# Optimization experiments

Measured on AMD Instinct MI355X. Metric: run time of the kernel, lower is better.

The kernel has to match this reference:

```python
import jax, jax.numpy as jnp
import numpy as np
import math

NH, NKV, D = 32, 8, 128  # query heads, kv heads, head_dim
ROPE_THETA = 10000.0


def _rotate_half(x):
    x1, x2 = jnp.split(x, 2, axis=-1)
    return jnp.concatenate([-x2, x1], axis=-1)


def _rope_cache(position_ids):
    # position_ids: [B, S] int -> cos, sin: [B, S, D]
    inv_freq = 1.0 / (ROPE_THETA ** (jnp.arange(0, D, 2, dtype=jnp.float32) / D))
    freqs = position_ids.astype(jnp.float32)[..., None] * inv_freq  # [B,S,D/2]
    emb = jnp.concatenate([freqs, freqs], axis=-1)  # [B,S,D]
    return jnp.cos(emb), jnp.sin(emb)


def setup_inputs() -> dict:
    key = jax.random.key(0)
    k0, k1, k2, k3, k4 = jax.random.split(key, 5)
    B, S, H = 1, 2048, 4096
    scale = 0.02
    return {
        "hidden_states": jax.random.normal(k0, (B, S, H), jnp.float32),
        "position_ids": jnp.broadcast_to(jnp.arange(S, dtype=jnp.int32), (B, S)),
        "Wq": jax.random.normal(k1, (H, NH * D), jnp.float32) * scale,
        "Wk": jax.random.normal(k2, (H, NKV * D), jnp.float32) * scale,
        "Wv": jax.random.normal(k3, (H, NKV * D), jnp.float32) * scale,
        "Wo": jax.random.normal(k4, (NH * D, H), jnp.float32) * scale,
    }


def reference(hidden_states, position_ids, Wq, Wk, Wv, Wo):
    B, S, H = hidden_states.shape
    # QKV projections, move heads front: [B, H, S, D]
    Q = (hidden_states @ Wq).reshape(B, S, NH, D).transpose(0, 2, 1, 3)
    K = (hidden_states @ Wk).reshape(B, S, NKV, D).transpose(0, 2, 1, 3)
    V = (hidden_states @ Wv).reshape(B, S, NKV, D).transpose(0, 2, 1, 3)
    # RoPE
    cos, sin = _rope_cache(position_ids)  # [B,S,D]
    cos, sin = cos[:, None], sin[:, None]  # broadcast over heads
    Q = Q * cos + _rotate_half(Q) * sin
    K = K * cos + _rotate_half(K) * sin
    # GQA: repeat kv heads to match query heads
    g = NH // NKV
    K = jnp.repeat(K, g, axis=1)
    V = jnp.repeat(V, g, axis=1)
    # scaled QK^T with causal mask (mask=True -> keep, else finfo.min)
    scores = jnp.einsum("bhqd,bhkd->bhqk", Q, K) / math.sqrt(D)
    causal = jnp.tril(jnp.ones((S, S), dtype=bool))
    scores = jnp.where(causal, scores, jnp.finfo(scores.dtype).min)
    probs = jax.nn.softmax(scores.astype(jnp.float32), axis=-1).astype(Q.dtype)
    attn = jnp.einsum("bhqk,bhkd->bhqd", probs, V)
    attn = attn.transpose(0, 2, 1, 3).reshape(B, S, NH * D)
    return attn @ Wo
```

## Files before the change

### kernel.cpp

```cpp
#include <hip/hip_runtime.h>
#include <hip/hip_bf16.h>
#include <math.h>

typedef __bf16 bf16;
typedef __bf16 bf16x4 __attribute__((ext_vector_type(4)));
typedef __bf16 bf16x8 __attribute__((ext_vector_type(8)));
typedef float f32x4 __attribute__((ext_vector_type(4)));

#define GLB __attribute__((address_space(1)))
#define LDSAS __attribute__((address_space(3)))

__global__ void probe_dtype(const unsigned int* __restrict__ X, int* __restrict__ flag) {
  int t = threadIdx.x;
  int cnt = 0;
  for (int i = t; i < 512; i += 64) {
    unsigned int e = (X[i] >> 7) & 0xFF;
    cnt += (e >= 110 && e <= 135) ? 1 : 0;
  }
#pragma unroll
  for (int off = 32; off > 0; off >>= 1) cnt += __shfl_down(cnt, off, 64);
  if (t == 0) flag[0] = (cnt < 256) ? 1 : 0;
}

__global__ void prep_weights(const void* __restrict__ Wq, const void* __restrict__ Wk,
                             const void* __restrict__ Wv, const void* __restrict__ Wo,
                             const void* __restrict__ X,
                             bf16* __restrict__ Wqkvt, bf16* __restrict__ Wot,
                             bf16* __restrict__ Xb, const int* __restrict__ flag) {
  const int f = flag[0];
  const int t = threadIdx.x;
  int b = blockIdx.x;
  __shared__ __attribute__((aligned(16))) bf16 tileT[64][72];
  const void* W;
  bf16* out;
  int N, bx, by;
  if (b < 4096) {
    W = Wq; out = Wqkvt; N = 4096; bx = b & 63; by = b >> 6;
  } else if (b < 5120) {
    b -= 4096; W = Wk; out = Wqkvt + (size_t)4096 * 4096; N = 1024; bx = b & 15; by = b >> 4;
  } else if (b < 6144) {
    b -= 5120; W = Wv; out = Wqkvt + (size_t)5120 * 4096; N = 1024; bx = b & 15; by = b >> 4;
  } else if (b < 10240) {
    b -= 6144; W = Wo; out = Wot; N = 4096; bx = b & 63; by = b >> 6;
  } else {
    b -= 10240;
    const size_t i = ((size_t)b * 256 + t) * 4;
    bf16x4 o;
    if (f) {
      const float4 v = *(const float4*)((const float*)X + i);
      o[0] = (bf16)v.x; o[1] = (bf16)v.y; o[2] = (bf16)v.z; o[3] = (bf16)v.w;
    } else {
      o = *(const bf16x4*)((const bf16*)X + i);
    }
    *(bf16x4*)&Xb[i] = o;
    return;
  }
  const int n0 = bx * 64, k0 = by * 64;

  const int rr = t >> 4, cc = (t & 15) * 4;
  const int s_in = (t & 15) >> 1;
#pragma unroll
  for (int p = 0; p < 4; ++p) {
    const int r = p * 16 + rr;
    bf16 vals[4];
    if (f) {
      const float4 v = *(const float4*)((const float*)W + (size_t)(k0 + r) * N + n0 + cc);
      vals[0] = (bf16)v.x; vals[1] = (bf16)v.y; vals[2] = (bf16)v.z; vals[3] = (bf16)v.w;
    } else {
      const bf16x4 v = *(const bf16x4*)((const bf16*)W + (size_t)(k0 + r) * N + n0 + cc);
#pragma unroll
      for (int u = 0; u < 4; ++u) vals[u] = v[u];
    }
    const int idx = (((r >> 3) ^ s_in) << 3) + (r & 7);
#pragma unroll
    for (int u = 0; u < 4; ++u) tileT[cc + u][idx] = vals[u];
  }
  __syncthreads();

  const int nn = t >> 3, c8 = t & 7;
#pragma unroll
  for (int p = 0; p < 2; ++p) {
    const int n = p * 32 + nn;
    const int s = (n >> 3) & 7;
    const bf16x8 v = *(const bf16x8*)&tileT[n][(c8 ^ s) * 8];
    *(bf16x8*)&out[(size_t)(n0 + n) * 4096 + k0 + c8 * 8] = v;
  }
}

__global__ __launch_bounds__(256, 2) void gemm_bt(
    const bf16* __restrict__ A, const bf16* __restrict__ Bt,
    void* __restrict__ C, const int* __restrict__ flagp, int M, int N, int K) {
  __shared__ bf16 As[128 * 32];
  __shared__ bf16 Bs[128 * 32];
  const int t = threadIdx.x;
  const int m0 = blockIdx.y * 128, n0 = blockIdx.x * 128;
  const int lane = t & 63, n16 = lane & 15, quad = lane >> 4;
  const int w = t >> 6, wrow = w >> 1, wcol = w & 1;

  f32x4 acc[4][4] = {};
  const int colA = (((t & 3) ^ ((t >> 3) & 3))) * 8;
  const int rA = t >> 2;
  const int sw = (n16 >> 1) & 3;
  const int rdoff = ((quad ^ sw) * 8);

  for (int k0 = 0; k0 < K; k0 += 32) {
#pragma unroll
    for (int i = 0; i < 2; ++i) {
      const int elem = i * 2048 + t * 8;
      const int row = i * 64 + rA;
      __builtin_amdgcn_global_load_lds(
          (const GLB void*)(A + (size_t)(m0 + row) * K + k0 + colA),
          (LDSAS void*)(&As[elem]), 16, 0, 0);
      __builtin_amdgcn_global_load_lds(
          (const GLB void*)(Bt + (size_t)(n0 + row) * K + k0 + colA),
          (LDSAS void*)(&Bs[elem]), 16, 0, 0);
    }
    __syncthreads();
    bf16x8 af[4], bfr[4];
#pragma unroll
    for (int i = 0; i < 4; ++i) {
      af[i] = *(const bf16x8*)&As[(wrow * 64 + i * 16 + n16) * 32 + rdoff];
      bfr[i] = *(const bf16x8*)&Bs[(wcol * 64 + i * 16 + n16) * 32 + rdoff];
    }
#pragma unroll
    for (int mi = 0; mi < 4; ++mi)
#pragma unroll
      for (int ni = 0; ni < 4; ++ni)
        acc[mi][ni] = __builtin_amdgcn_mfma_f32_16x16x32_bf16(
            af[mi], bfr[ni], acc[mi][ni], 0, 0, 0);
    __syncthreads();
  }
  const bool f32out = (flagp != nullptr) && (flagp[0] != 0);
  if (f32out) {
    float* Cf = (float*)C;
#pragma unroll
    for (int mi = 0; mi < 4; ++mi)
#pragma unroll
      for (int ni = 0; ni < 4; ++ni) {
        const int r0 = m0 + wrow * 64 + mi * 16 + quad * 4;
        const int c = n0 + wcol * 64 + ni * 16 + n16;
#pragma unroll
        for (int r = 0; r < 4; ++r) Cf[(size_t)(r0 + r) * N + c] = acc[mi][ni][r];
      }
  } else {
    bf16* Cb = (bf16*)C;
#pragma unroll
    for (int mi = 0; mi < 4; ++mi)
#pragma unroll
      for (int ni = 0; ni < 4; ++ni) {
        const int r0 = m0 + wrow * 64 + mi * 16 + quad * 4;
        const int c = n0 + wcol * 64 + ni * 16 + n16;
#pragma unroll
        for (int r = 0; r < 4; ++r) Cb[(size_t)(r0 + r) * N + c] = (bf16)acc[mi][ni][r];
      }
  }
}

__global__ void rope_vt(bf16* __restrict__ QKV, const int* __restrict__ pos,
                        bf16* __restrict__ Vt) {
  const int t = threadIdx.x;
  int b = blockIdx.x;
  if (b < 20480) {
    const int idx = b * 256 + t;
    const int i = idx & 63;
    const int hh = (idx >> 6) % 40;
    const int s = idx / (64 * 40);
    bf16* px = QKV + (size_t)s * 6144 + hh * 128 + i;
    const float x1 = (float)px[0], x2 = (float)px[64];
    const float p = (float)pos[s];
    const float inv = exp2f((float)i * -0.2076205088f);
    float sn, cs;
    sincosf(p * inv, &sn, &cs);
    px[0] = (bf16)(x1 * cs - x2 * sn);
    px[64] = (bf16)(x2 * cs + x1 * sn);
  } else {
    b -= 20480;
    __shared__ bf16 tile[32][34];
    const int tx = t & 31, ty = t >> 5;
    const int v0 = (b & 31) * 32, s0 = (b >> 5) * 32;
#pragma unroll
    for (int j = 0; j < 4; ++j)
      tile[ty + j * 8][tx] = QKV[(size_t)(s0 + ty + j * 8) * 6144 + 5120 + v0 + tx];
    __syncthreads();
#pragma unroll
    for (int j = 0; j < 4; ++j)
      Vt[(size_t)(v0 + ty + j * 8) * 2048 + s0 + tx] = tile[tx][ty + j * 8];
  }
}

__global__ __launch_bounds__(256) void flash_attn(
    const bf16* __restrict__ QKV, const bf16* __restrict__ Vt_g,
    bf16* __restrict__ O) {
  __shared__ bf16 Ks[2][64 * 128];
  __shared__ bf16 Vs[2][128 * 64];
  __shared__ bf16 Ps[64 * 72];
  const int pairp = blockIdx.x;
  const int h = blockIdx.y, hkv = h >> 2;
  const int t = threadIdx.x, w = t >> 6, lane = t & 63;
  const int n16 = lane & 15, quad = lane >> 4;
  const bf16* Qp = QKV + h * 128;
  const bf16* Kp = QKV + 4096 + hkv * 128;
  const bf16* Vp = Vt_g + (size_t)hkv * 128 * 2048;

  const int krow = t >> 4, kg = t & 15;
  const int vd = t >> 3, vg = t & 7;

  for (int pass = 0; pass < 2; ++pass) {
    const int qt = (pass == 0) ? pairp : 31 - pairp;
    bf16x8 qa[4];
    {
      const bf16* qrow = Qp + (size_t)(qt * 64 + w * 16 + n16) * 6144 + quad * 8;
#pragma unroll
      for (int kf = 0; kf < 4; ++kf) qa[kf] = *(const bf16x8*)(qrow + kf * 32);
    }
    f32x4 o[8] = {};
    float l_ = 0.f;

    __syncthreads();

    auto stage = [&](int kt, int buf) {
#pragma unroll
      for (int j = 0; j < 4; ++j) {
        const int row = j * 16 + krow;
        const int g = kg ^ (row & 7);
        __builtin_amdgcn_global_load_lds(
            (const GLB void*)(Kp + (size_t)(kt * 64 + row) * 6144 + g * 8),
            (LDSAS void*)(&Ks[buf][j * 2048 + t * 8]), 16, 0, 0);
      }
#pragma unroll
      for (int j = 0; j < 4; ++j) {
        const int d = j * 32 + vd;
        const int g = vg ^ (d & 7);
        __builtin_amdgcn_global_load_lds(
            (const GLB void*)(Vp + (size_t)d * 2048 + kt * 64 + g * 8),
            (LDSAS void*)(&Vs[buf][j * 2048 + t * 8]), 16, 0, 0);
      }
    };

    stage(0, 0);
    for (int kt = 0; kt <= qt; ++kt) {
      const int cur = kt & 1;
      __syncthreads();
      if (kt < qt) stage(kt + 1, cur ^ 1);

      const bool diag = (kt == qt);
      const int s7 = n16 & 7;
      const int qloc = w * 16 + n16;
#pragma unroll
      for (int ns = 0; ns < 4; ++ns) {
        f32x4 c = {};
        __builtin_amdgcn_s_setprio(1);
#pragma unroll
        for (int kf = 0; kf < 4; ++kf)
          c = __builtin_amdgcn_mfma_f32_16x16x32_bf16(
              *(const bf16x8*)&Ks[cur][(ns * 16 + n16) * 128 +
                                       (((kf * 4 + quad) ^ s7) * 8)],
              qa[kf], c, 0, 0, 0);
        __builtin_amdgcn_s_setprio(0);
        float p[4];
        if (diag) {
          const int kv0 = ns * 16 + quad * 4;
#pragma unroll
          for (int r = 0; r < 4; ++r)
            p[r] = (kv0 + r > qloc)
                       ? 0.f
                       : __expf(fminf(c[r] * 0.08838834764831845f, 60.f));
        } else {
#pragma unroll
          for (int r = 0; r < 4; ++r)
            p[r] = __expf(fminf(c[r] * 0.08838834764831845f, 60.f));
        }
        l_ += (p[0] + p[1]) + (p[2] + p[3]);
        bf16x4 pb;
#pragma unroll
        for (int r = 0; r < 4; ++r) pb[r] = (bf16)p[r];
        *(bf16x4*)&Ps[(size_t)qloc * 72 + ns * 16 + quad * 4] = pb;
      }
      const bf16x8 a0 = *(const bf16x8*)&Ps[(w * 16 + n16) * 72 + quad * 8];
      const bf16x8 a1 = *(const bf16x8*)&Ps[(w * 16 + n16) * 72 + 32 + quad * 8];
      __builtin_amdgcn_s_setprio(1);
#pragma unroll
      for (int dt = 0; dt < 8; ++dt) {
        const int d = dt * 16 + n16;
        const bf16x8 b0 = *(const bf16x8*)&Vs[cur][d * 64 + ((quad ^ s7) * 8)];
        o[dt] = __builtin_amdgcn_mfma_f32_16x16x32_bf16(a0, b0, o[dt], 0, 0, 0);
        const bf16x8 b1 = *(const bf16x8*)&Vs[cur][d * 64 + (((4 + quad) ^ s7) * 8)];
        o[dt] = __builtin_amdgcn_mfma_f32_16x16x32_bf16(a1, b1, o[dt], 0, 0, 0);
      }
      __builtin_amdgcn_s_setprio(0);
    }
    l_ += __shfl_xor(l_, 16, 64);
    l_ += __shfl_xor(l_, 32, 64);
    float linv[4];
#pragma unroll
    for (int r = 0; r < 4; ++r) linv[r] = 1.f / __shfl(l_, quad * 4 + r, 64);
#pragma unroll
    for (int dt = 0; dt < 8; ++dt)
#pragma unroll
      for (int r = 0; r < 4; ++r) {
        const int qi = qt * 64 + w * 16 + quad * 4 + r;
        O[(size_t)qi * 4096 + h * 128 + dt * 16 + n16] = (bf16)(o[dt][r] * linv[r]);
      }
  }
}

extern "C" void kernel_launch(void* const* d_in, const int* in_sizes, int n_in,
                              void* d_out, int out_size, void* d_ws, size_t ws_size,
                              hipStream_t stream) {
  (void)in_sizes; (void)n_in; (void)out_size; (void)ws_size;
  const void* X = d_in[0];
  const int* pos = (const int*)d_in[1];
  const void* Wq = d_in[2];
  const void* Wk = d_in[3];
  const void* Wv = d_in[4];
  const void* Wo = d_in[5];

  char* ws = (char*)d_ws;
  const size_t MB = 1ull << 20;
  int* flag   = (int*)(ws + 0);
  bf16* Xb    = (bf16*)(ws + 1 * MB);
  bf16* attn  = (bf16*)(ws + 1 * MB);
  bf16* Wqkvt = (bf16*)(ws + 17 * MB);
  bf16* Wot   = (bf16*)(ws + 65 * MB);
  bf16* QKV   = (bf16*)(ws + 97 * MB);
  bf16* Vt_g  = (bf16*)(ws + 121 * MB);

  probe_dtype<<<1, 64, 0, stream>>>((const unsigned int*)X, flag);

  prep_weights<<<18432, 256, 0, stream>>>(Wq, Wk, Wv, Wo, X, Wqkvt, Wot, Xb, flag);

  gemm_bt<<<dim3(48, 16), 256, 0, stream>>>(Xb, Wqkvt, QKV, nullptr, 2048, 6144, 4096);

  rope_vt<<<22528, 256, 0, stream>>>(QKV, pos, Vt_g);

  flash_attn<<<dim3(16, 32), 256, 0, stream>>>(QKV, Vt_g, attn);

  gemm_bt<<<dim3(32, 16), 256, 0, stream>>>(attn, Wot, d_out, flag, 2048, 4096, 4096);
}
```

Baseline: 490.9 us.

## Halve flash-attention KV tile, remap blocks by KV head, batch RoPE per token

Flash attention now stages 32-key K/V tiles instead of 64, which cuts shared memory so more blocks fit per CU (launch bounds raised to 4). Causal masking is redone for the finer tiles, and the V layout drops its XOR swizzle. Blocks are remapped so that query heads sharing a KV head run close together in launch order, which should improve cache reuse. RoPE now computes sin/cos once per token and position and loops over the 40 heads, using far fewer blocks. The risks are doubled loop and sync overhead per key and possible LDS bank conflicts on unswizzled V reads.

```diff
diff --git a/kernel.cpp b/kernel.cpp
--- a/kernel.cpp
+++ b/kernel.cpp
@@ -160,21 +160,23 @@
                         bf16* __restrict__ Vt) {
   const int t = threadIdx.x;
   int b = blockIdx.x;
-  if (b < 20480) {
-    const int idx = b * 256 + t;
-    const int i = idx & 63;
-    const int hh = (idx >> 6) % 40;
-    const int s = idx / (64 * 40);
-    bf16* px = QKV + (size_t)s * 6144 + hh * 128 + i;
-    const float x1 = (float)px[0], x2 = (float)px[64];
+  if (b < 512) {
+    const int i = t & 63;
+    const int s = b * 4 + (t >> 6);
     const float p = (float)pos[s];
     const float inv = exp2f((float)i * -0.2076205088f);
     float sn, cs;
     sincosf(p * inv, &sn, &cs);
-    px[0] = (bf16)(x1 * cs - x2 * sn);
-    px[64] = (bf16)(x2 * cs + x1 * sn);
+    bf16* base = QKV + (size_t)s * 6144 + i;
+#pragma unroll 4
+    for (int hh = 0; hh < 40; ++hh) {
+      bf16* px = base + hh * 128;
+      const float x1 = (float)px[0], x2 = (float)px[64];
+      px[0] = (bf16)(x1 * cs - x2 * sn);
+      px[64] = (bf16)(x2 * cs + x1 * sn);
+    }
   } else {
-    b -= 20480;
+    b -= 512;
     __shared__ bf16 tile[32][34];
     const int tx = t & 31, ty = t >> 5;
     const int v0 = (b & 31) * 32, s0 = (b >> 5) * 32;
@@ -188,14 +190,17 @@
   }
 }
 
-__global__ __launch_bounds__(256) void flash_attn(
+__global__ __launch_bounds__(256, 4) void flash_attn(
     const bf16* __restrict__ QKV, const bf16* __restrict__ Vt_g,
     bf16* __restrict__ O) {
-  __shared__ bf16 Ks[2][64 * 128];
-  __shared__ bf16 Vs[2][128 * 64];
-  __shared__ bf16 Ps[64 * 72];
-  const int pairp = blockIdx.x;
-  const int h = blockIdx.y, hkv = h >> 2;
+  __shared__ bf16 Ks[2][32 * 128];
+  __shared__ bf16 Vs[2][128 * 32];
+  __shared__ bf16 Ps[64 * 48];
+  const int flat = blockIdx.y * 16 + blockIdx.x;
+  const int m = flat >> 3;
+  const int h = (flat & 7) * 4 + (m >> 4);
+  const int pairp = m & 15;
+  const int hkv = h >> 2;
   const int t = threadIdx.x, w = t >> 6, lane = t & 63;
   const int n16 = lane & 15, quad = lane >> 4;
   const bf16* Qp = QKV + h * 128;
@@ -203,7 +208,7 @@
   const bf16* Vp = Vt_g + (size_t)hkv * 128 * 2048;
 
   const int krow = t >> 4, kg = t & 15;
-  const int vd = t >> 3, vg = t & 7;
+  const int vd = t >> 2, vg = t & 3;
 
   for (int pass = 0; pass < 2; ++pass) {
     const int qt = (pass == 0) ? pairp : 31 - pairp;
@@ -220,34 +225,35 @@
 
     auto stage = [&](int kt, int buf) {
 #pragma unroll
-      for (int j = 0; j < 4; ++j) {
+      for (int j = 0; j < 2; ++j) {
         const int row = j * 16 + krow;
         const int g = kg ^ (row & 7);
         __builtin_amdgcn_global_load_lds(
-            (const GLB void*)(Kp + (size_t)(kt * 64 + row) * 6144 + g * 8),
+            (const GLB void*)(Kp + (size_t)(kt * 32 + row) * 6144 + g * 8),
             (LDSAS void*)(&Ks[buf][j * 2048 + t * 8]), 16, 0, 0);
       }
 #pragma unroll
-      for (int j = 0; j < 4; ++j) {
-        const int d = j * 32 + vd;
-        const int g = vg ^ (d & 7);
+      for (int j = 0; j < 2; ++j) {
+        const int d = j * 64 + vd;
         __builtin_amdgcn_global_load_lds(
-            (const GLB void*)(Vp + (size_t)d * 2048 + kt * 64 + g * 8),
+            (const GLB void*)(Vp + (size_t)d * 2048 + kt * 32 + vg * 8),
             (LDSAS void*)(&Vs[buf][j * 2048 + t * 8]), 16, 0, 0);
       }
     };
 
+    const int nk = 2 * qt + 2;
     stage(0, 0);
-    for (int kt = 0; kt <= qt; ++kt) {
+    for (int kt = 0; kt < nk; ++kt) {
       const int cur = kt & 1;
       __syncthreads();
-      if (kt < qt) stage(kt + 1, cur ^ 1);
-
-      const bool diag = (kt == qt);
+      if (kt + 1 < nk) stage(kt + 1, cur ^ 1);
+
+      const bool diag = (kt >= 2 * qt);
+      const int dof = kt * 32 - qt * 64;
       const int s7 = n16 & 7;
       const int qloc = w * 16 + n16;
 #pragma unroll
-      for (int ns = 0; ns < 4; ++ns) {
+      for (int ns = 0; ns < 2; ++ns) {
         f32x4 c = {};
         __builtin_amdgcn_s_setprio(1);
 #pragma unroll
@@ -259,7 +265,7 @@
         __builtin_amdgcn_s_setprio(0);
         float p[4];
         if (diag) {
-          const int kv0 = ns * 16 + quad * 4;
+          const int kv0 = dof + ns * 16 + quad * 4;
 #pragma unroll
           for (int r = 0; r < 4; ++r)
             p[r] = (kv0 + r > qloc)
@@ -274,18 +280,15 @@
         bf16x4 pb;
 #pragma unroll
         for (int r = 0; r < 4; ++r) pb[r] = (bf16)p[r];
-        *(bf16x4*)&Ps[(size_t)qloc * 72 + ns * 16 + quad * 4] = pb;
-      }
-      const bf16x8 a0 = *(const bf16x8*)&Ps[(w * 16 + n16) * 72 + quad * 8];
-      const bf16x8 a1 = *(const bf16x8*)&Ps[(w * 16 + n16) * 72 + 32 + quad * 8];
+        *(bf16x4*)&Ps[(size_t)qloc * 48 + ns * 16 + quad * 4] = pb;
+      }
+      const bf16x8 a0 = *(const bf16x8*)&Ps[(w * 16 + n16) * 48 + quad * 8];
       __builtin_amdgcn_s_setprio(1);
 #pragma unroll
       for (int dt = 0; dt < 8; ++dt) {
         const int d = dt * 16 + n16;
-        const bf16x8 b0 = *(const bf16x8*)&Vs[cur][d * 64 + ((quad ^ s7) * 8)];
+        const bf16x8 b0 = *(const bf16x8*)&Vs[cur][d * 32 + quad * 8];
         o[dt] = __builtin_amdgcn_mfma_f32_16x16x32_bf16(a0, b0, o[dt], 0, 0, 0);
-        const bf16x8 b1 = *(const bf16x8*)&Vs[cur][d * 64 + (((4 + quad) ^ s7) * 8)];
-        o[dt] = __builtin_amdgcn_mfma_f32_16x16x32_bf16(a1, b1, o[dt], 0, 0, 0);
       }
       __builtin_amdgcn_s_setprio(0);
     }
@@ -331,7 +334,7 @@
 
   gemm_bt<<<dim3(48, 16), 256, 0, stream>>>(Xb, Wqkvt, QKV, nullptr, 2048, 6144, 4096);
 
-  rope_vt<<<22528, 256, 0, stream>>>(QKV, pos, Vt_g);
+  rope_vt<<<2560, 256, 0, stream>>>(QKV, pos, Vt_g);
 
   flash_attn<<<dim3(16, 32), 256, 0, stream>>>(QKV, Vt_g, attn);
 
```

Result: no change. 494.5 us (+0.7%).
